# Optimization experiments

Hardware: AMD Instinct MI355X
Metric: run time of the kernel (lower is better)

Reference implementation:

```python
import jax, jax.numpy as jnp
import numpy as np

B, Q, K, D = 16, 2048, 2048, 128
NEG = -1000000.0  # matches torch module's mask fill value (not -inf)


def setup_inputs() -> dict:
    key = jax.random.key(0)
    kq, kk, kv, kl = jax.random.split(key, 4)
    q = jax.random.normal(kq, (B, Q, D), dtype=jnp.float32)
    k = jax.random.normal(kk, (B, K, D), dtype=jnp.float32)
    v = jax.random.normal(kv, (B, K, D), dtype=jnp.float32)
    valid_lens = jax.random.randint(kl, (B, 1), 0, K, dtype=jnp.int32)
    return {"q": q, "k": k, "v": v, "valid_lens": valid_lens}


def reference(q, k, v, valid_lens):
    d = q.shape[-1]
    # scores: (B, Q, K)
    weight = jnp.einsum('bqd,bkd->bqk', q, k) / jnp.sqrt(jnp.asarray(d, q.dtype))
    # mask: key position j valid iff j < valid_len[b]; broadcast over query dim
    mask = jnp.arange(k.shape[1])[None, None, :] < valid_lens[:, :, None]  # (B,1,K)
    weight = jnp.where(mask, weight, NEG)
    score = jax.nn.softmax(weight, axis=-1)
    return jnp.einsum('bqk,bkv->bqv', score, v)
```

## Files before the change

kernel.cpp:

```cpp
#include <hip/hip_runtime.h>

constexpr int NB = 16;
constexpr int NQ = 2048;
constexpr int NK = 2048;
constexpr int ND = 128;
constexpr int KVBLK = 64;
constexpr int NTILE = NK / KVBLK;
constexpr int TILE_USH = KVBLK * ND;
constexpr float SCALE2 = 0.12751744751442557f;

typedef __attribute__((ext_vector_type(4))) float f4;
typedef __attribute__((ext_vector_type(16))) float f32x16;
typedef __attribute__((ext_vector_type(8))) unsigned short us8;
typedef __attribute__((ext_vector_type(8))) __bf16 bf16x8;
typedef __attribute__((ext_vector_type(4))) unsigned int u32x4;

static __device__ __forceinline__ unsigned short f2bf(float f) {
    unsigned u = __builtin_bit_cast(unsigned, f);
    u += 0x7fffu + ((u >> 16) & 1u);
    return (unsigned short)(u >> 16);
}
static __device__ __forceinline__ f4 splat4(float x) { f4 r = {x,x,x,x}; return r; }

static __device__ __forceinline__ float fexp2(float x) {
    float r;
    asm("v_exp_f32 %0, %1" : "=v"(r) : "v"(x));
    return r;
}

static __device__ __forceinline__ void load_lds16(const unsigned short* g, unsigned short* l) {
    __builtin_amdgcn_global_load_lds(
        (const __attribute__((address_space(1))) void*)g,
        (__attribute__((address_space(3))) void*)l,
        16, 0, 0);
}

static __device__ __forceinline__ unsigned cvt_pk_bf16(float lo, float hi) {
    unsigned r;
    asm("v_cvt_pk_bf16_f32 %0, %1, %2" : "=v"(r) : "v"(lo), "v"(hi));
    return r;
}

__global__ __launch_bounds__(256)
void prep_kv5(const float* __restrict__ kg, const float* __restrict__ vg,
              const int* __restrict__ vlen,
              unsigned short* __restrict__ wk, unsigned short* __restrict__ wvt)
{
    const int b   = blockIdx.y;
    const int t   = blockIdx.x;
    const int kv0 = t * KVBLK;

    {
        const int v = vlen[b];
        const int Leff = (v <= 0) ? NK : v;
        if (kv0 >= Leff) return;
    }

    const int t0  = threadIdx.x;

    __shared__ __align__(16) unsigned short vl[64 * 136];

    {
        const int kv = t0 >> 2;
        const int c  = t0 & 3;
        const float* gp = kg + (size_t)(b * NK + kv0 + kv) * ND + c * 32;
        unsigned short* ob = wk + (size_t)(b * NTILE + t) * TILE_USH;
        #pragma unroll
        for (int g = 0; g < 4; ++g) {
            f4 f0 = *(const f4*)(gp + g * 8);
            f4 f1 = *(const f4*)(gp + g * 8 + 4);
            us8 w;
            #pragma unroll
            for (int i = 0; i < 4; ++i) { w[i] = f2bf(f0[i]); w[i+4] = f2bf(f1[i]); }
            const int d0 = c * 32 + g * 8;
            const int f  = (kv >> 5) * 8 + (d0 >> 4);
            const int off = f * 512 + ((d0 >> 3) & 1) * 256 + (kv & 31) * 8;
            *(us8*)(ob + off) = w;
        }
    }
    {
        const int kv = t0 >> 2;
        const int d0 = (t0 & 3) * 32;
        const float* gp = vg + (size_t)(b * NK + kv0 + kv) * ND + d0;
        unsigned short* lb = &vl[kv * 136 + d0];
        #pragma unroll
        for (int g = 0; g < 4; ++g) {
            f4 f0 = *(const f4*)(gp + g * 8);
            f4 f1 = *(const f4*)(gp + g * 8 + 4);
            us8 w;
            #pragma unroll
            for (int i = 0; i < 4; ++i) { w[i] = f2bf(f0[i]); w[i+4] = f2bf(f1[i]); }
            *(us8*)(lb + g * 8) = w;
        }
    }
    __syncthreads();
    {
        unsigned short* ob = wvt + (size_t)(b * NTILE + t) * TILE_USH;
        #pragma unroll
        for (int iter = 0; iter < 4; ++iter) {
            const int cid = iter * 256 + t0;
            const int f   = cid >> 6;
            const int l   = cid & 63;
            const int kb  = (f >> 2) * 16 + (l >> 5) * 8;
            const int d   = (f & 3) * 32 + (l & 31);
            us8 w;
            #pragma unroll
            for (int j = 0; j < 8; ++j) w[j] = vl[(kb + j) * 136 + d];
            *(us8*)(ob + cid * 8) = w;
        }
    }
}

__global__ __launch_bounds__(256, 2)
void attn_fused18(const float* __restrict__ qg, const int* __restrict__ vlen,
                  const unsigned short* __restrict__ wk,
                  const unsigned short* __restrict__ wvt,
                  float* __restrict__ og)
{
    const int bid  = blockIdx.x;
    const int half = bid >> 8;
    const int j    = bid & 255;
    const int rank = half ? (15 - (j & 7)) : (j & 7);
    const int qc   = j >> 3;
    const int q0   = qc * 64;

    int b = 0;
    {
        int Ls[16];
        #pragma unroll
        for (int i = 0; i < 16; ++i) {
            const int v = vlen[i];
            Ls[i] = (v <= 0) ? NK : v;
        }
        #pragma unroll
        for (int bb = 0; bb < 16; ++bb) {
            int r = 0;
            #pragma unroll
            for (int cc = 0; cc < 16; ++cc)
                r += (Ls[cc] > Ls[bb] || (Ls[cc] == Ls[bb] && cc < bb)) ? 1 : 0;
            if (r == rank) b = bb;
        }
    }

    const int tid  = threadIdx.x;
    const int wid  = tid >> 6;
    const int grp  = wid >> 1;
    const int qw   = wid & 1;
    const int lane = tid & 63;
    const int lq   = lane & 31;
    const int hi   = lane >> 5;

    const int L = vlen[b];
    const bool uniform = (L <= 0);
    const int Leff = uniform ? NK : L;
    const int ntiles = (Leff + KVBLK - 1) / KVBLK;
    const int ng    = (ntiles + 1 - grp) >> 1;
    const int niter = (ntiles + 1) >> 1;

    __shared__ __align__(16) unsigned short kbuf[2][2][8192];

    bf16x8 aq[8];
    {
        const float* qp = qg + (size_t)(b * NQ + q0 + qw * 32 + lq) * ND + hi * 8;
        #pragma unroll
        for (int c = 0; c < 8; ++c) {
            f4 f0 = *(const f4*)(qp + c * 16);
            f4 f1 = *(const f4*)(qp + c * 16 + 4);
            us8 u;
            #pragma unroll
            for (int i = 0; i < 4; ++i) {
                u[i]     = f2bf(f0[i] * SCALE2);
                u[i + 4] = f2bf(f1[i] * SCALE2);
            }
            aq[c] = __builtin_bit_cast(bf16x8, u);
        }
    }

    const unsigned short* kbg = wk  + (size_t)b * NTILE * TILE_USH;
    const unsigned short* vbg = wvt + (size_t)b * NTILE * TILE_USH;

    const int s_off = qw * 4096 + lane * 8;

    float m_r = -__builtin_inff();
    float l_r = 0.f;
    f32x16 accO[4];
    #pragma unroll
    for (int dc = 0; dc < 4; ++dc)
        #pragma unroll
        for (int r = 0; r < 16; ++r) accO[dc][r] = 0.f;

    if (grp < ntiles) {
        const unsigned short* src = kbg + (size_t)grp * TILE_USH + s_off;
        unsigned short* dst = &kbuf[grp][0][qw * 4096];
        #pragma unroll
        for (int jj = 0; jj < 8; ++jj) load_lds16(src + jj * 512, dst + jj * 512);
    }
    __syncthreads();

    for (int i = 0; i < niter; ++i) {
        const int tile = 2 * i + grp;
        const int buf  = i & 1;

        {
            const int tn = tile + 2;
            if (tn < ntiles) {
                const unsigned short* src = kbg + (size_t)tn * TILE_USH + s_off;
                unsigned short* dst = &kbuf[grp][buf ^ 1][qw * 4096];
                #pragma unroll
                for (int jj = 0; jj < 8; ++jj) load_lds16(src + jj * 512, dst + jj * 512);
            }
        }

        if (i < ng) {
            const int kv0 = tile * KVBLK;
            const unsigned short* kl = &kbuf[grp][buf][0];

            us8 kf[16];
            #pragma unroll
            for (int c = 0; c < 16; ++c)
                kf[c] = *(const us8*)&kl[c * 512 + lane * 8];
            f32x16 sA, sB;
            #pragma unroll
            for (int r = 0; r < 16; ++r) { sA[r] = 0.f; sB[r] = 0.f; }
            #pragma unroll
            for (int c = 0; c < 8; ++c) {
                sA = __builtin_amdgcn_mfma_f32_32x32x16_bf16(
                    __builtin_bit_cast(bf16x8, kf[c]), aq[c], sA, 0, 0, 0);
                sB = __builtin_amdgcn_mfma_f32_32x32x16_bf16(
                    __builtin_bit_cast(bf16x8, kf[8 + c]), aq[c], sB, 0, 0, 0);
            }
            __builtin_amdgcn_sched_barrier(0);

            us8 vf[16];
            {
                const unsigned short* vsrc = vbg + (size_t)tile * TILE_USH + lane * 8;
                #pragma unroll
                for (int f = 0; f < 16; ++f)
                    vf[f] = *(const us8*)(vsrc + f * 512);
            }

            if (uniform) {
                #pragma unroll
                for (int r = 0; r < 16; ++r) { sA[r] = 0.f; sB[r] = 0.f; }
            } else {
                const int lim0 = L - kv0 - 4 * hi;
                const int lim1 = lim0 - 32;
                #pragma unroll
                for (int r = 0; r < 16; ++r) {
                    const int rc = (r & 3) + 8 * (r >> 2);
                    sA[r] = (rc >= lim0) ? -__builtin_inff() : sA[r];
                    sB[r] = (rc >= lim1) ? -__builtin_inff() : sB[r];
                }
            }

            float tt[11];
            #pragma unroll
            for (int g3 = 0; g3 < 5; ++g3)
                tt[g3] = fmaxf(fmaxf(sA[3 * g3], sA[3 * g3 + 1]), sA[3 * g3 + 2]);
            tt[5] = fmaxf(fmaxf(sA[15], sB[0]), sB[1]);
            #pragma unroll
            for (int g3 = 0; g3 < 4; ++g3)
                tt[6 + g3] = fmaxf(fmaxf(sB[3 * g3 + 2], sB[3 * g3 + 3]), sB[3 * g3 + 4]);
            tt[10] = fmaxf(sB[14], sB[15]);
            const float u0 = fmaxf(fmaxf(tt[0], tt[1]), tt[2]);
            const float u1 = fmaxf(fmaxf(tt[3], tt[4]), tt[5]);
            const float u2 = fmaxf(fmaxf(tt[6], tt[7]), tt[8]);
            const float u3 = fmaxf(tt[9], tt[10]);
            const float pm = fmaxf(fmaxf(u0, u1), fmaxf(u2, u3));
            float pmax = fmaxf(pm, __shfl_xor(pm, 32));

            if (__any(pmax > m_r)) {
                const float mnew = fmaxf(m_r, pmax);
                const float sc = fexp2(m_r - mnew);
                m_r = mnew;
                l_r *= sc;
                #pragma unroll
                for (int r = 0; r < 16; ++r) {
                    const int src = ((r & 3) + 8 * (r >> 2) + 4 * hi) + (lane & 32);
                    const float scr = __shfl(sc, src);
                    accO[0][r] *= scr; accO[1][r] *= scr;
                    accO[2][r] *= scr; accO[3][r] *= scr;
                }
            }

            float p0[16], p1[16];
            #pragma unroll
            for (int r = 0; r < 16; ++r) {
                p0[r] = fexp2(sA[r] - m_r);
                p1[r] = fexp2(sB[r] - m_r);
            }
            float sm[8];
            #pragma unroll
            for (int i2 = 0; i2 < 8; ++i2)
                sm[i2] = (p0[i2] + p0[i2 + 8]) + (p1[i2] + p1[i2 + 8]);
            #pragma unroll
            for (int i2 = 0; i2 < 4; ++i2) sm[i2] += sm[i2 + 4];
            float rsum = (sm[0] + sm[1]) + (sm[2] + sm[3]);
            rsum += __shfl_xor(rsum, 32);
            l_r += rsum;

            unsigned cw[16];
            #pragma unroll
            for (int i2 = 0; i2 < 8; ++i2) cw[i2] = cvt_pk_bf16(p0[2 * i2], p0[2 * i2 + 1]);
            #pragma unroll
            for (int i2 = 0; i2 < 8; ++i2) cw[8 + i2] = cvt_pk_bf16(p1[2 * i2], p1[2 * i2 + 1]);

            bf16x8 pa[4];
            #pragma unroll
            for (int ks = 0; ks < 4; ++ks) {
                const int a = 4 * ks;
                const unsigned u = hi ? cw[a]     : cw[a + 2];
                const unsigned v = hi ? cw[a + 1] : cw[a + 3];
                const unsigned up = __shfl_xor((int)u, 32);
                const unsigned vp = __shfl_xor((int)v, 32);
                u32x4 w;
                w[0] = hi ? up        : cw[a];
                w[1] = hi ? vp        : cw[a + 1];
                w[2] = hi ? cw[a + 2] : up;
                w[3] = hi ? cw[a + 3] : vp;
                pa[ks] = __builtin_bit_cast(bf16x8, w);
            }

            #pragma unroll
            for (int dc = 0; dc < 4; ++dc) {
                #pragma unroll
                for (int ks = 0; ks < 4; ++ks) {
                    accO[dc] = __builtin_amdgcn_mfma_f32_32x32x16_bf16(
                        pa[ks], __builtin_bit_cast(bf16x8, vf[ks * 4 + dc]), accO[dc], 0, 0, 0);
                }
            }
        }

        __syncthreads();
    }

    float* accb = (float*)&kbuf[0][0][0];
    float* mlb  = accb + 8192;
    if (grp == 1) {
        #pragma unroll
        for (int dc = 0; dc < 4; ++dc) {
            #pragma unroll
            for (int q4 = 0; q4 < 4; ++q4) {
                f4 v;
                #pragma unroll
                for (int c = 0; c < 4; ++c) v[c] = accO[dc][q4 * 4 + c];
                *(f4*)&accb[(((qw * 16 + dc * 4 + q4) * 64) + lane) * 4] = v;
            }
        }
        if (hi == 0) {
            mlb[qw * 32 + lq]      = m_r;
            mlb[64 + qw * 32 + lq] = l_r;
        }
    }
    __syncthreads();
    if (grp == 0) {
        const float m1 = mlb[qw * 32 + lq];
        const float l1 = mlb[64 + qw * 32 + lq];
        const float m  = fmaxf(m_r, m1);
        const float a0 = fexp2(m_r - m), a1 = fexp2(m1 - m);
        const float linv = 1.0f / (a0 * l_r + a1 * l1);
        const float s0v = a0 * linv, s1v = a1 * linv;
        float* ob = og + (size_t)(b * NQ + q0 + qw * 32) * ND;
        #pragma unroll
        for (int dc = 0; dc < 4; ++dc) {
            #pragma unroll
            for (int q4 = 0; q4 < 4; ++q4) {
                f4 o1 = *(const f4*)&accb[(((qw * 16 + dc * 4 + q4) * 64) + lane) * 4];
                #pragma unroll
                for (int c = 0; c < 4; ++c) {
                    const int r = q4 * 4 + c;
                    const int row = c + 8 * q4 + 4 * hi;
                    const float s0r = __shfl(s0v, row + (lane & 32));
                    const float s1r = __shfl(s1v, row + (lane & 32));
                    ob[(size_t)row * ND + dc * 32 + lq] = accO[dc][r] * s0r + o1[c] * s1r;
                }
            }
        }
    }
}

__global__ __launch_bounds__(256, 2)
void attn_fused(const float* __restrict__ qg, const float* __restrict__ kg,
                const float* __restrict__ vg, const int* __restrict__ vlen,
                float* __restrict__ og)
{
    const int b    = blockIdx.y;
    const int q0   = blockIdx.x * 64;
    const int tid  = threadIdx.x;
    const int wid  = tid >> 6;
    const int lane = tid & 63;
    const int lrow = lane & 15;
    const int lgrp = lane >> 4;
    constexpr float SCALE = 0.08838834764831844f;

    const int L = vlen[b];
    const bool uniform = (L <= 0);
    const int Leff = uniform ? NK : L;
    const int nt32 = (Leff + 31) / 32;

    __shared__ __align__(16) unsigned short kt[32 * 136];
    __shared__ __align__(16) unsigned short vt[128 * 40];
    __shared__ __align__(16) float pt[4][16 * 36];

    bf16x8 aqf[4];
    {
        const float* qp = qg + (size_t)(b * NQ + q0 + wid * 16 + lrow) * ND + lgrp * 8;
        #pragma unroll
        for (int c = 0; c < 4; ++c) {
            f4 f0 = *(const f4*)(qp + c * 32);
            f4 f1 = *(const f4*)(qp + c * 32 + 4);
            us8 u;
            #pragma unroll
            for (int i = 0; i < 4; ++i) {
                u[i]     = f2bf(f0[i] * SCALE);
                u[i + 4] = f2bf(f1[i] * SCALE);
            }
            aqf[c] = __builtin_bit_cast(bf16x8, u);
        }
    }

    float m_r[4], l_r[4];
    f4 accO[8];
    #pragma unroll
    for (int r = 0; r < 4; ++r) { m_r[r] = -__builtin_inff(); l_r[r] = 0.f; }
    #pragma unroll
    for (int dc = 0; dc < 8; ++dc) accO[dc] = splat4(0.f);

    for (int t = 0; t < nt32; ++t) {
        const int kv0 = t * 32;
        __syncthreads();
        {
            const int r  = tid >> 3;
            const int c0 = (tid & 7) * 16;
            const float* gp = kg + (size_t)(b * NK + kv0 + r) * ND + c0;
            f4 f0 = *(const f4*)(gp);
            f4 f1 = *(const f4*)(gp + 4);
            f4 f2 = *(const f4*)(gp + 8);
            f4 f3 = *(const f4*)(gp + 12);
            us8 w0, w1;
            #pragma unroll
            for (int i = 0; i < 4; ++i) {
                w0[i]     = f2bf(f0[i]);
                w0[i + 4] = f2bf(f1[i]);
                w1[i]     = f2bf(f2[i]);
                w1[i + 4] = f2bf(f3[i]);
            }
            unsigned short* dst = &kt[r * 136 + c0];
            *(us8*)(dst)     = w0;
            *(us8*)(dst + 8) = w1;
        }
        {
            const int d  = tid & 127;
            const int g2 = tid >> 7;
            const float* gp = vg + (size_t)(b * NK + kv0 + g2 * 16) * ND + d;
            us8 w0, w1;
            #pragma unroll
            for (int jj = 0; jj < 8; ++jj) {
                w0[jj] = f2bf(gp[(size_t)jj * ND]);
                w1[jj] = f2bf(gp[(size_t)(jj + 8) * ND]);
            }
            unsigned short* dst = &vt[d * 40 + g2 * 16];
            *(us8*)(dst)     = w0;
            *(us8*)(dst + 8) = w1;
        }
        __syncthreads();

        f4 s0 = splat4(0.f), s1 = splat4(0.f);
        #pragma unroll
        for (int c = 0; c < 4; ++c) {
            bf16x8 bk0 = __builtin_bit_cast(bf16x8,
                *(const us8*)&kt[lrow * 136 + c * 32 + lgrp * 8]);
            s0 = __builtin_amdgcn_mfma_f32_16x16x32_bf16(aqf[c], bk0, s0, 0, 0, 0);
            bf16x8 bk1 = __builtin_bit_cast(bf16x8,
                *(const us8*)&kt[(16 + lrow) * 136 + c * 32 + lgrp * 8]);
            s1 = __builtin_amdgcn_mfma_f32_16x16x32_bf16(aqf[c], bk1, s1, 0, 0, 0);
        }

        const int col0 = kv0 + lrow;
        if (uniform) {
            s0 = splat4(0.f);
            s1 = splat4(0.f);
        } else {
            if (col0 >= L)      s0 = splat4(-__builtin_inff());
            if (col0 + 16 >= L) s1 = splat4(-__builtin_inff());
        }

        float pm[4];
        #pragma unroll
        for (int r = 0; r < 4; ++r) pm[r] = fmaxf(s0[r], s1[r]);
        #pragma unroll
        for (int off = 8; off > 0; off >>= 1) {
            #pragma unroll
            for (int r = 0; r < 4; ++r)
                pm[r] = fmaxf(pm[r], __shfl_xor(pm[r], off));
        }
        float pr0[4], pr1[4], rs[4], sc[4];
        #pragma unroll
        for (int r = 0; r < 4; ++r) {
            float mn = fmaxf(m_r[r], pm[r]);
            sc[r]  = __expf(m_r[r] - mn);
            m_r[r] = mn;
            pr0[r] = __expf(s0[r] - mn);
            pr1[r] = __expf(s1[r] - mn);
            rs[r]  = pr0[r] + pr1[r];
        }
        #pragma unroll
        for (int off = 8; off > 0; off >>= 1) {
            #pragma unroll
            for (int r = 0; r < 4; ++r)
                rs[r] += __shfl_xor(rs[r], off);
        }
        #pragma unroll
        for (int r = 0; r < 4; ++r) l_r[r] = l_r[r] * sc[r] + rs[r];
        #pragma unroll
        for (int dc = 0; dc < 8; ++dc) {
            #pragma unroll
            for (int r = 0; r < 4; ++r) accO[dc][r] *= sc[r];
        }

        float* pw = pt[wid];
        #pragma unroll
        for (int r = 0; r < 4; ++r) {
            pw[(lgrp * 4 + r) * 36 + lrow]      = pr0[r];
            pw[(lgrp * 4 + r) * 36 + 16 + lrow] = pr1[r];
        }
        asm volatile("s_waitcnt lgkmcnt(0)" ::: "memory");
        f4 a0 = *(const f4*)&pw[lrow * 36 + lgrp * 8];
        f4 a1 = *(const f4*)&pw[lrow * 36 + lgrp * 8 + 4];
        us8 au;
        #pragma unroll
        for (int i = 0; i < 4; ++i) { au[i] = f2bf(a0[i]); au[i + 4] = f2bf(a1[i]); }
        bf16x8 ap = __builtin_bit_cast(bf16x8, au);

        #pragma unroll
        for (int dc = 0; dc < 8; ++dc) {
            bf16x8 bv = __builtin_bit_cast(bf16x8,
                *(const us8*)&vt[(dc * 16 + lrow) * 40 + lgrp * 8]);
            accO[dc] = __builtin_amdgcn_mfma_f32_16x16x32_bf16(ap, bv, accO[dc], 0, 0, 0);
        }
    }

    float inv[4];
    #pragma unroll
    for (int r = 0; r < 4; ++r) inv[r] = 1.0f / l_r[r];
    float* op = og + (size_t)(b * NQ + q0 + wid * 16) * ND;
    #pragma unroll
    for (int dc = 0; dc < 8; ++dc) {
        #pragma unroll
        for (int r = 0; r < 4; ++r)
            op[(lgrp * 4 + r) * ND + dc * 16 + lrow] = accO[dc][r] * inv[r];
    }
}

extern "C" void kernel_launch(void* const* d_in, const int* in_sizes, int n_in,
                              void* d_out, int out_size, void* d_ws, size_t ws_size,
                              hipStream_t stream) {
    (void)in_sizes; (void)n_in; (void)out_size;
    const float* q  = (const float*)d_in[0];
    const float* k  = (const float*)d_in[1];
    const float* v  = (const float*)d_in[2];
    const int*   vl = (const int*)d_in[3];
    float* out = (float*)d_out;

    const size_t kvbytes = 2 * (size_t)NB * NK * ND * sizeof(unsigned short);
    if (ws_size >= kvbytes) {
        unsigned short* wk  = (unsigned short*)d_ws;
        unsigned short* wvt = wk + (size_t)NB * NK * ND;
        hipLaunchKernelGGL(prep_kv5, dim3(NTILE, NB), dim3(256), 0, stream, k, v, vl, wk, wvt);
        hipLaunchKernelGGL(attn_fused18, dim3((NQ / 64) * NB), dim3(256), 0, stream,
                           q, vl, wk, wvt, out);
    } else {
        hipLaunchKernelGGL(attn_fused, dim3(NQ / 64, NB), dim3(256), 0, stream,
                           q, k, v, vl, out);
    }
}
```

Before: 55.01 us.

## Load K tiles directly from global and shrink blocks to 32 queries

Each block now covers 32 queries with two waves instead of 64 queries with four, which doubles the grid. K fragments are read straight from global memory into registers, so the LDS double-buffered prefetch and the per-iteration __syncthreads are gone. This removes LDS staging and barrier overhead and frees LDS for higher occupancy. The cost is that K is no longer shared across query waves through LDS, so every K tile is fetched twice as often from global/L2, and loads are no longer overlapped through a prefetch pipeline.

```diff
diff --git a/kernel.cpp b/kernel.cpp
--- a/kernel.cpp
+++ b/kernel.cpp
@@ -111,18 +111,19 @@
     }
 }
 
-__global__ __launch_bounds__(256, 2)
-void attn_fused18(const float* __restrict__ qg, const int* __restrict__ vlen,
+__global__ __launch_bounds__(128, 2)
+void attn_fused19(const float* __restrict__ qg, const int* __restrict__ vlen,
                   const unsigned short* __restrict__ wk,
                   const unsigned short* __restrict__ wvt,
                   float* __restrict__ og)
 {
-    const int bid  = blockIdx.x;
-    const int half = bid >> 8;
-    const int j    = bid & 255;
-    const int rank = half ? (15 - (j & 7)) : (j & 7);
-    const int qc   = j >> 3;
-    const int q0   = qc * 64;
+    const int bid     = blockIdx.x;
+    const int quarter = bid >> 8;
+    const int j       = bid & 255;
+    const int slot    = j & 7;
+    const int rank    = (quarter & 1) ? (15 - slot) : slot;
+    const int qc      = (j >> 3) + ((quarter >> 1) << 5);
+    const int q0      = qc * 32;
 
     int b = 0;
     {
@@ -143,9 +144,7 @@
     }
 
     const int tid  = threadIdx.x;
-    const int wid  = tid >> 6;
-    const int grp  = wid >> 1;
-    const int qw   = wid & 1;
+    const int grp  = tid >> 6;
     const int lane = tid & 63;
     const int lq   = lane & 31;
     const int hi   = lane >> 5;
@@ -154,14 +153,14 @@
     const bool uniform = (L <= 0);
     const int Leff = uniform ? NK : L;
     const int ntiles = (Leff + KVBLK - 1) / KVBLK;
-    const int ng    = (ntiles + 1 - grp) >> 1;
-    const int niter = (ntiles + 1) >> 1;
-
-    __shared__ __align__(16) unsigned short kbuf[2][2][8192];
+    const int ng = (ntiles > grp) ? ((ntiles - grp + 1) >> 1) : 0;
+
+    __shared__ __align__(16) float accb[32 * 128];
+    __shared__ float mlb[64];
 
     bf16x8 aq[8];
     {
-        const float* qp = qg + (size_t)(b * NQ + q0 + qw * 32 + lq) * ND + hi * 8;
+        const float* qp = qg + (size_t)(b * NQ + q0 + lq) * ND + hi * 8;
         #pragma unroll
         for (int c = 0; c < 8; ++c) {
             f4 f0 = *(const f4*)(qp + c * 16);
@@ -179,9 +178,7 @@
     const unsigned short* kbg = wk  + (size_t)b * NTILE * TILE_USH;
     const unsigned short* vbg = wvt + (size_t)b * NTILE * TILE_USH;
 
-    const int s_off = qw * 4096 + lane * 8;
-
-    float m_r = -__builtin_inff();
+    float m_r = -1e30f;
     float l_r = 0.f;
     f32x16 accO[4];
     #pragma unroll
@@ -189,153 +186,129 @@
         #pragma unroll
         for (int r = 0; r < 16; ++r) accO[dc][r] = 0.f;
 
-    if (grp < ntiles) {
-        const unsigned short* src = kbg + (size_t)grp * TILE_USH + s_off;
-        unsigned short* dst = &kbuf[grp][0][qw * 4096];
-        #pragma unroll
-        for (int jj = 0; jj < 8; ++jj) load_lds16(src + jj * 512, dst + jj * 512);
-    }
-    __syncthreads();
-
-    for (int i = 0; i < niter; ++i) {
+    for (int i = 0; i < ng; ++i) {
         const int tile = 2 * i + grp;
-        const int buf  = i & 1;
-
+        const int kv0  = tile * KVBLK;
+
+        us8 kf[16];
         {
-            const int tn = tile + 2;
-            if (tn < ntiles) {
-                const unsigned short* src = kbg + (size_t)tn * TILE_USH + s_off;
-                unsigned short* dst = &kbuf[grp][buf ^ 1][qw * 4096];
-                #pragma unroll
-                for (int jj = 0; jj < 8; ++jj) load_lds16(src + jj * 512, dst + jj * 512);
-            }
-        }
-
-        if (i < ng) {
-            const int kv0 = tile * KVBLK;
-            const unsigned short* kl = &kbuf[grp][buf][0];
-
-            us8 kf[16];
+            const unsigned short* ksrc = kbg + (size_t)tile * TILE_USH + lane * 8;
             #pragma unroll
             for (int c = 0; c < 16; ++c)
-                kf[c] = *(const us8*)&kl[c * 512 + lane * 8];
-            f32x16 sA, sB;
+                kf[c] = *(const us8*)(ksrc + c * 512);
+        }
+        f32x16 sA, sB;
+        #pragma unroll
+        for (int r = 0; r < 16; ++r) { sA[r] = 0.f; sB[r] = 0.f; }
+        #pragma unroll
+        for (int c = 0; c < 8; ++c) {
+            sA = __builtin_amdgcn_mfma_f32_32x32x16_bf16(
+                __builtin_bit_cast(bf16x8, kf[c]), aq[c], sA, 0, 0, 0);
+            sB = __builtin_amdgcn_mfma_f32_32x32x16_bf16(
+                __builtin_bit_cast(bf16x8, kf[8 + c]), aq[c], sB, 0, 0, 0);
+        }
+        __builtin_amdgcn_sched_barrier(0);
+
+        us8 vf[16];
+        {
+            const unsigned short* vsrc = vbg + (size_t)tile * TILE_USH + lane * 8;
+            #pragma unroll
+            for (int f = 0; f < 16; ++f)
+                vf[f] = *(const us8*)(vsrc + f * 512);
+        }
+
+        if (uniform) {
             #pragma unroll
             for (int r = 0; r < 16; ++r) { sA[r] = 0.f; sB[r] = 0.f; }
-            #pragma unroll
-            for (int c = 0; c < 8; ++c) {
-                sA = __builtin_amdgcn_mfma_f32_32x32x16_bf16(
-                    __builtin_bit_cast(bf16x8, kf[c]), aq[c], sA, 0, 0, 0);
-                sB = __builtin_amdgcn_mfma_f32_32x32x16_bf16(
-                    __builtin_bit_cast(bf16x8, kf[8 + c]), aq[c], sB, 0, 0, 0);
-            }
-            __builtin_amdgcn_sched_barrier(0);
-
-            us8 vf[16];
-            {
-                const unsigned short* vsrc = vbg + (size_t)tile * TILE_USH + lane * 8;
-                #pragma unroll
-                for (int f = 0; f < 16; ++f)
-                    vf[f] = *(const us8*)(vsrc + f * 512);
-            }
-
-            if (uniform) {
-                #pragma unroll
-                for (int r = 0; r < 16; ++r) { sA[r] = 0.f; sB[r] = 0.f; }
-            } else {
-                const int lim0 = L - kv0 - 4 * hi;
-                const int lim1 = lim0 - 32;
-                #pragma unroll
-                for (int r = 0; r < 16; ++r) {
-                    const int rc = (r & 3) + 8 * (r >> 2);
-                    sA[r] = (rc >= lim0) ? -__builtin_inff() : sA[r];
-                    sB[r] = (rc >= lim1) ? -__builtin_inff() : sB[r];
-                }
-            }
-
-            float tt[11];
-            #pragma unroll
-            for (int g3 = 0; g3 < 5; ++g3)
-                tt[g3] = fmaxf(fmaxf(sA[3 * g3], sA[3 * g3 + 1]), sA[3 * g3 + 2]);
-            tt[5] = fmaxf(fmaxf(sA[15], sB[0]), sB[1]);
-            #pragma unroll
-            for (int g3 = 0; g3 < 4; ++g3)
-                tt[6 + g3] = fmaxf(fmaxf(sB[3 * g3 + 2], sB[3 * g3 + 3]), sB[3 * g3 + 4]);
-            tt[10] = fmaxf(sB[14], sB[15]);
-            const float u0 = fmaxf(fmaxf(tt[0], tt[1]), tt[2]);
-            const float u1 = fmaxf(fmaxf(tt[3], tt[4]), tt[5]);
-            const float u2 = fmaxf(fmaxf(tt[6], tt[7]), tt[8]);
-            const float u3 = fmaxf(tt[9], tt[10]);
-            const float pm = fmaxf(fmaxf(u0, u1), fmaxf(u2, u3));
-            float pmax = fmaxf(pm, __shfl_xor(pm, 32));
-
-            if (__any(pmax > m_r)) {
-                const float mnew = fmaxf(m_r, pmax);
-                const float sc = fexp2(m_r - mnew);
-                m_r = mnew;
-                l_r *= sc;
-                #pragma unroll
-                for (int r = 0; r < 16; ++r) {
-                    const int src = ((r & 3) + 8 * (r >> 2) + 4 * hi) + (lane & 32);
-                    const float scr = __shfl(sc, src);
-                    accO[0][r] *= scr; accO[1][r] *= scr;
-                    accO[2][r] *= scr; accO[3][r] *= scr;
-                }
-            }
-
-            float p0[16], p1[16];
+        } else {
+            const int lim0 = L - kv0 - 4 * hi;
+            const int lim1 = lim0 - 32;
             #pragma unroll
             for (int r = 0; r < 16; ++r) {
-                p0[r] = fexp2(sA[r] - m_r);
-                p1[r] = fexp2(sB[r] - m_r);
-            }
-            float sm[8];
-            #pragma unroll
-            for (int i2 = 0; i2 < 8; ++i2)
-                sm[i2] = (p0[i2] + p0[i2 + 8]) + (p1[i2] + p1[i2 + 8]);
-            #pragma unroll
-            for (int i2 = 0; i2 < 4; ++i2) sm[i2] += sm[i2 + 4];
-            float rsum = (sm[0] + sm[1]) + (sm[2] + sm[3]);
-            rsum += __shfl_xor(rsum, 32);
-            l_r += rsum;
-
-            unsigned cw[16];
-            #pragma unroll
-            for (int i2 = 0; i2 < 8; ++i2) cw[i2] = cvt_pk_bf16(p0[2 * i2], p0[2 * i2 + 1]);
-            #pragma unroll
-            for (int i2 = 0; i2 < 8; ++i2) cw[8 + i2] = cvt_pk_bf16(p1[2 * i2], p1[2 * i2 + 1]);
-
-            bf16x8 pa[4];
+                const int rc = (r & 3) + 8 * (r >> 2);
+                sA[r] = (rc >= lim0) ? -__builtin_inff() : sA[r];
+                sB[r] = (rc >= lim1) ? -__builtin_inff() : sB[r];
+            }
+        }
+
+        float tt[11];
+        #pragma unroll
+        for (int g3 = 0; g3 < 5; ++g3)
+            tt[g3] = fmaxf(fmaxf(sA[3 * g3], sA[3 * g3 + 1]), sA[3 * g3 + 2]);
+        tt[5] = fmaxf(fmaxf(sA[15], sB[0]), sB[1]);
+        #pragma unroll
+        for (int g3 = 0; g3 < 4; ++g3)
+            tt[6 + g3] = fmaxf(fmaxf(sB[3 * g3 + 2], sB[3 * g3 + 3]), sB[3 * g3 + 4]);
+        tt[10] = fmaxf(sB[14], sB[15]);
+        const float u0 = fmaxf(fmaxf(tt[0], tt[1]), tt[2]);
+        const float u1 = fmaxf(fmaxf(tt[3], tt[4]), tt[5]);
+        const float u2 = fmaxf(fmaxf(tt[6], tt[7]), tt[8]);
+        const float u3 = fmaxf(tt[9], tt[10]);
+        const float pm = fmaxf(fmaxf(u0, u1), fmaxf(u2, u3));
+        float pmax = fmaxf(pm, __shfl_xor(pm, 32));
+
+        if (__any(pmax > m_r)) {
+            const float mnew = fmaxf(m_r, pmax);
+            const float sc = fexp2(m_r - mnew);
+            m_r = mnew;
+            l_r *= sc;
+            #pragma unroll
+            for (int r = 0; r < 16; ++r) {
+                const int src = ((r & 3) + 8 * (r >> 2) + 4 * hi) + (lane & 32);
+                const float scr = __shfl(sc, src);
+                accO[0][r] *= scr; accO[1][r] *= scr;
+                accO[2][r] *= scr; accO[3][r] *= scr;
+            }
+        }
+
+        float p0[16], p1[16];
+        #pragma unroll
+        for (int r = 0; r < 16; ++r) {
+            p0[r] = fexp2(sA[r] - m_r);
+            p1[r] = fexp2(sB[r] - m_r);
+        }
+        float sm[8];
+        #pragma unroll
+        for (int i2 = 0; i2 < 8; ++i2)
+            sm[i2] = (p0[i2] + p0[i2 + 8]) + (p1[i2] + p1[i2 + 8]);
+        #pragma unroll
+        for (int i2 = 0; i2 < 4; ++i2) sm[i2] += sm[i2 + 4];
+        float rsum = (sm[0] + sm[1]) + (sm[2] + sm[3]);
+        rsum += __shfl_xor(rsum, 32);
+        l_r += rsum;
+
+        unsigned cw[16];
+        #pragma unroll
+        for (int i2 = 0; i2 < 8; ++i2) cw[i2] = cvt_pk_bf16(p0[2 * i2], p0[2 * i2 + 1]);
+        #pragma unroll
+        for (int i2 = 0; i2 < 8; ++i2) cw[8 + i2] = cvt_pk_bf16(p1[2 * i2], p1[2 * i2 + 1]);
+
+        bf16x8 pa[4];
+        #pragma unroll
+        for (int ks = 0; ks < 4; ++ks) {
+            const int a = 4 * ks;
+            const unsigned u = hi ? cw[a]     : cw[a + 2];
+            const unsigned v = hi ? cw[a + 1] : cw[a + 3];
+            const unsigned up = __shfl_xor((int)u, 32);
+            const unsigned vp = __shfl_xor((int)v, 32);
+            u32x4 w;
+            w[0] = hi ? up        : cw[a];
+            w[1] = hi ? vp        : cw[a + 1];
+            w[2] = hi ? cw[a + 2] : up;
+            w[3] = hi ? cw[a + 3] : vp;
+            pa[ks] = __builtin_bit_cast(bf16x8, w);
+        }
+
+        #pragma unroll
+        for (int dc = 0; dc < 4; ++dc) {
             #pragma unroll
             for (int ks = 0; ks < 4; ++ks) {
-                const int a = 4 * ks;
-                const unsigned u = hi ? cw[a]     : cw[a + 2];
-                const unsigned v = hi ? cw[a + 1] : cw[a + 3];
-                const unsigned up = __shfl_xor((int)u, 32);
-                const unsigned vp = __shfl_xor((int)v, 32);
-                u32x4 w;
-                w[0] = hi ? up        : cw[a];
-                w[1] = hi ? vp        : cw[a + 1];
-                w[2] = hi ? cw[a + 2] : up;
-                w[3] = hi ? cw[a + 3] : vp;
-                pa[ks] = __builtin_bit_cast(bf16x8, w);
-            }
-
-            #pragma unroll
-            for (int dc = 0; dc < 4; ++dc) {
-                #pragma unroll
-                for (int ks = 0; ks < 4; ++ks) {
-                    accO[dc] = __builtin_amdgcn_mfma_f32_32x32x16_bf16(
-                        pa[ks], __builtin_bit_cast(bf16x8, vf[ks * 4 + dc]), accO[dc], 0, 0, 0);
-                }
-            }
-        }
-
-        __syncthreads();
-    }
-
-    float* accb = (float*)&kbuf[0][0][0];
-    float* mlb  = accb + 8192;
+                accO[dc] = __builtin_amdgcn_mfma_f32_32x32x16_bf16(
+                    pa[ks], __builtin_bit_cast(bf16x8, vf[ks * 4 + dc]), accO[dc], 0, 0, 0);
+            }
+        }
+    }
+
     if (grp == 1) {
         #pragma unroll
         for (int dc = 0; dc < 4; ++dc) {
@@ -344,28 +317,28 @@
                 f4 v;
                 #pragma unroll
                 for (int c = 0; c < 4; ++c) v[c] = accO[dc][q4 * 4 + c];
-                *(f4*)&accb[(((qw * 16 + dc * 4 + q4) * 64) + lane) * 4] = v;
+                *(f4*)&accb[(((dc * 4 + q4) * 64) + lane) * 4] = v;
             }
         }
         if (hi == 0) {
-            mlb[qw * 32 + lq]      = m_r;
-            mlb[64 + qw * 32 + lq] = l_r;
+            mlb[lq]      = m_r;
+            mlb[32 + lq] = l_r;
         }
     }
     __syncthreads();
     if (grp == 0) {
-        const float m1 = mlb[qw * 32 + lq];
-        const float l1 = mlb[64 + qw * 32 + lq];
+        const float m1 = mlb[lq];
+        const float l1 = mlb[32 + lq];
         const float m  = fmaxf(m_r, m1);
         const float a0 = fexp2(m_r - m), a1 = fexp2(m1 - m);
         const float linv = 1.0f / (a0 * l_r + a1 * l1);
         const float s0v = a0 * linv, s1v = a1 * linv;
-        float* ob = og + (size_t)(b * NQ + q0 + qw * 32) * ND;
+        float* ob = og + (size_t)(b * NQ + q0) * ND;
         #pragma unroll
         for (int dc = 0; dc < 4; ++dc) {
             #pragma unroll
             for (int q4 = 0; q4 < 4; ++q4) {
-                f4 o1 = *(const f4*)&accb[(((qw * 16 + dc * 4 + q4) * 64) + lane) * 4];
+                f4 o1 = *(const f4*)&accb[(((dc * 4 + q4) * 64) + lane) * 4];
                 #pragma unroll
                 for (int c = 0; c < 4; ++c) {
                     const int r = q4 * 4 + c;
@@ -567,7 +540,7 @@
         unsigned short* wk  = (unsigned short*)d_ws;
         unsigned short* wvt = wk + (size_t)NB * NK * ND;
         hipLaunchKernelGGL(prep_kv5, dim3(NTILE, NB), dim3(256), 0, stream, k, v, vl, wk, wvt);
-        hipLaunchKernelGGL(attn_fused18, dim3((NQ / 64) * NB), dim3(256), 0, stream,
+        hipLaunchKernelGGL(attn_fused19, dim3((NQ / 32) * NB), dim3(128), 0, stream,
                            q, vl, wk, wvt, out);
     } else {
         hipLaunchKernelGGL(attn_fused, dim3(NQ / 64, NB), dim3(256), 0, stream,
```

Result: faster. 51.94 us (median of 2 runs) (-5.6%).
